# Performance work log

Hardware: AMD Instinct MI355X
Metric: run time of the kernel (lower is better)

The kernel has to match this reference:

```python
import jax, jax.numpy as jnp
import numpy as np

N = 50000      # nodes
E = 1600000    # edges
IN = 128       # in_features
OUT = 64       # out_features
H = 2          # heads
ALPHA = 0.2    # LeakyReLU negative slope


def setup_inputs() -> dict:
    key = jax.random.key(0)
    k1, k2, k3, k4 = jax.random.split(key, 4)
    x = jax.random.normal(k1, (N, IN), dtype=jnp.float32)
    edge_index = jax.random.randint(k2, (2, E), 0, N, dtype=jnp.int32)
    # xavier-uniform-ish scaled params
    W = jax.random.normal(k3, (H, IN, OUT), dtype=jnp.float32) / np.float32(np.sqrt(IN))
    a = jax.random.normal(k4, (H, 2 * OUT, 1), dtype=jnp.float32) * np.float32(0.1)
    return {"x": x, "W": W, "a": a, "edge_index": edge_index}


def reference(x, W, a, edge_index):
    src = edge_index[0]
    dst = edge_index[1]
    # per-head linear transform: [N, H, O]
    Wh = jnp.einsum('ni,hio->nho', x, W)
    # split attention vector: a @ [Wh_i || Wh_j] == Wh_i@a_i + Wh_j@a_j
    a_i = a[:, :OUT, 0]   # [H, O]
    a_j = a[:, OUT:, 0]   # [H, O]
    s_i = jnp.einsum('nho,ho->nh', Wh, a_i)   # [N, H]
    s_j = jnp.einsum('nho,ho->nh', Wh, a_j)   # [N, H]
    # per-edge attention logits, LeakyReLU
    e = jax.nn.leaky_relu(s_i[src] + s_j[dst], negative_slope=ALPHA)  # [E, H]
    # faithful to source: GLOBAL softmax over all edges (dim=0) per head
    attn = jax.nn.softmax(e, axis=0)  # [E, H]
    # dropout with rate 0.0 -> identity (eval mode)
    msg = attn[:, :, None] * Wh[dst]  # [E, H, O]
    h = jax.ops.segment_sum(msg, dst, num_segments=N)  # [N, H, O]
    # concat heads along feature dim
    return h.reshape(N, H * OUT)
```

## Files before the change

### kernel.cpp

```cpp
#include <hip/hip_runtime.h>

#define NN 50000
#define EE 1600000
#define INF 128
#define OUTF 64
#define NH 2
#define ALPHA 0.2f

#define RNG 16
#define NPR (NN / RNG)
#define NBB 250
#define EPB (EE / NBB)
#define BCAP 640
#define NBNODE 391
#define HCH 25
#define SPB (NBB / HCH)

typedef __attribute__((ext_vector_type(8))) short s16x8;
typedef __attribute__((ext_vector_type(4))) float f32x4;

__device__ __forceinline__ unsigned short bf16_rne(float f) {
    union { float f; unsigned u; } v; v.f = f;
    unsigned r = v.u + 0x7FFFu + ((v.u >> 16) & 1u);
    return (unsigned short)(r >> 16);
}
__device__ __forceinline__ float bf16_val(unsigned short h) {
    union { unsigned u; float f; } v; v.u = ((unsigned)h) << 16;
    return v.f;
}
__device__ __forceinline__ void split8(const float4 a, const float4 b,
                                       s16x8& hi, s16x8& lo) {
    const float p[8] = {a.x, a.y, a.z, a.w, b.x, b.y, b.z, b.w};
    #pragma unroll
    for (int j = 0; j < 8; ++j) {
        const unsigned short h = bf16_rne(p[j]);
        hi[j] = (short)h;
        lo[j] = (short)bf16_rne(p[j] - bf16_val(h));
    }
}


__global__ __launch_bounds__(256)
void gat_wprep(const float* __restrict__ Wg, const float* __restrict__ a,
               unsigned short* __restrict__ Wf, float* __restrict__ Z)
{
    const int tid = threadIdx.x;
    const int idx = blockIdx.x * 256 + tid;
    if (idx < 2) Z[idx] = 0.0f;
    {
        const int h = idx >> 13;
        const int k = (idx >> 6) & 127;
        const int o = idx & 63;
        const float w = Wg[idx];
        const unsigned short hi = bf16_rne(w);
        const unsigned short lo = bf16_rne(w - bf16_val(hi));
        const int n  = h * 64 + o;
        const int nt = n >> 4;
        const int ks = k >> 5;
        const int kk = k & 31;
        const int ln = (kk >> 3) * 16 + (n & 15);
        const int pos = ((nt * 4 + ks) * 64 + ln) * 8 + (kk & 7);
        Wf[pos] = hi;
        Wf[18432 + pos] = lo;
    }
    if (blockIdx.x == 0) {
        for (int i = tid; i < 2048; i += 256) {
            Wf[16384 + i] = 0;
            Wf[18432 + 16384 + i] = 0;
        }
        __syncthreads();
        if (tid < 128) {
            const int k = tid;
            float u[4] = {0.f, 0.f, 0.f, 0.f};
            for (int o = 0; o < 64; ++o) {
                const float w0 = Wg[k * 64 + o];
                const float w1 = Wg[8192 + k * 64 + o];
                u[0] = fmaf(w0, a[o], u[0]);
                u[1] = fmaf(w0, a[64 + o], u[1]);
                u[2] = fmaf(w1, a[128 + o], u[2]);
                u[3] = fmaf(w1, a[192 + o], u[3]);
            }
            const int ks = k >> 5;
            const int kk = k & 31;
            #pragma unroll
            for (int n = 0; n < 4; ++n) {
                const int ln = (kk >> 3) * 16 + n;
                const int pos = ((32 + ks) * 64 + ln) * 8 + (kk & 7);
                const unsigned short hi = bf16_rne(u[n]);
                Wf[pos] = hi;
                Wf[18432 + pos] = bf16_rne(u[n] - bf16_val(hi));
            }
        }
    }
}

__global__ __launch_bounds__(256)
void gat_node(const float* __restrict__ x, const unsigned short* __restrict__ Wf,
              const int* __restrict__ ei, float* __restrict__ out,
              float* __restrict__ si, float* __restrict__ sj,
              unsigned* __restrict__ buckets, int* __restrict__ counts)
{
    __shared__ unsigned short WsL[36864];
    __shared__ int cnt[16];
    const int tid = threadIdx.x;

    if (blockIdx.x < NBB) {
        const int bid = blockIdx.x;
        if (tid < 16) cnt[tid] = 0;
        __syncthreads();
        const int e0 = bid * EPB;
        for (int i = tid; i < EPB / 4; i += 256) {
            const int4 s4 = *(const int4*)&ei[e0 + 4 * i];
            const int4 d4 = *(const int4*)&ei[EE + e0 + 4 * i];
            const int ss[4] = {s4.x, s4.y, s4.z, s4.w};
            const int dd[4] = {d4.x, d4.y, d4.z, d4.w};
            #pragma unroll
            for (int k = 0; k < 4; ++k) {
                const int r = dd[k] / NPR;
                const int rel = dd[k] - r * NPR;
                const int pos = atomicAdd(&cnt[r], 1);
                if (pos < BCAP)
                    buckets[(size_t)(r * NBB + bid) * BCAP + pos] =
                        (unsigned)ss[k] | ((unsigned)rel << 16);
            }
        }
        __syncthreads();
        if (tid < 16) counts[tid * NBB + bid] = min(cnt[tid], BCAP);
        return;
    }

    const int bx = blockIdx.x - NBB;
    const int lane = tid & 63;
    const int wv = tid >> 6;
    const int lm = lane & 15;
    const int quad = lane >> 4;

    {
        const float4* gsrc = (const float4*)Wf;
        float4* ldst = (float4*)WsL;
        #pragma unroll
        for (int i = 0; i < 18; ++i)
            ldst[i * 256 + tid] = gsrc[i * 256 + tid];
    }

    const int rowA0 = bx * 128 + wv * 32 + lm;
    const int rowA1 = rowA0 + 16;
    const int rc0 = rowA0 < NN ? rowA0 : NN - 1;
    const int rc1 = rowA1 < NN ? rowA1 : NN - 1;
    const float* xp0 = x + (size_t)rc0 * INF + quad * 8;
    const float* xp1 = x + (size_t)rc1 * INF + quad * 8;

    f32x4 acc[2][9];
    #pragma unroll
    for (int mi = 0; mi < 2; ++mi)
        #pragma unroll
        for (int nt = 0; nt < 9; ++nt) acc[mi][nt] = (f32x4)0.0f;

    __syncthreads();

    #pragma unroll
    for (int ks = 0; ks < 4; ++ks) {
        s16x8 ah0, al0, ah1, al1;
        {
            const float4 u0 = *(const float4*)(xp0 + ks * 32);
            const float4 v0 = *(const float4*)(xp0 + ks * 32 + 4);
            split8(u0, v0, ah0, al0);
            const float4 u1 = *(const float4*)(xp1 + ks * 32);
            const float4 v1 = *(const float4*)(xp1 + ks * 32 + 4);
            split8(u1, v1, ah1, al1);
        }
        #pragma unroll
        for (int nt = 0; nt < 9; ++nt) {
            const s16x8 bh = *(const s16x8*)&WsL[((nt * 4 + ks) * 64 + lane) * 8];
            const s16x8 bl = *(const s16x8*)&WsL[18432 + ((nt * 4 + ks) * 64 + lane) * 8];
            acc[0][nt] = __builtin_amdgcn_mfma_f32_16x16x32_bf16(ah0, bh, acc[0][nt], 0, 0, 0);
            acc[0][nt] = __builtin_amdgcn_mfma_f32_16x16x32_bf16(ah0, bl, acc[0][nt], 0, 0, 0);
            acc[0][nt] = __builtin_amdgcn_mfma_f32_16x16x32_bf16(al0, bh, acc[0][nt], 0, 0, 0);
            acc[1][nt] = __builtin_amdgcn_mfma_f32_16x16x32_bf16(ah1, bh, acc[1][nt], 0, 0, 0);
            acc[1][nt] = __builtin_amdgcn_mfma_f32_16x16x32_bf16(ah1, bl, acc[1][nt], 0, 0, 0);
            acc[1][nt] = __builtin_amdgcn_mfma_f32_16x16x32_bf16(al1, bh, acc[1][nt], 0, 0, 0);
        }
    }

    #pragma unroll
    for (int mi = 0; mi < 2; ++mi) {
        const int rowb = bx * 128 + wv * 32 + mi * 16 + quad * 4;
        #pragma unroll
        for (int r = 0; r < 4; ++r) {
            const int rr = rowb + r;
            if (rr < NN) {
                const float sv = acc[mi][8][r];
                if (lm == 0)      si[2 * rr] = sv;
                else if (lm == 1) sj[2 * rr] = sv;
                else if (lm == 2) si[2 * rr + 1] = sv;
                else if (lm == 3) sj[2 * rr + 1] = sv;
                float* orow = out + (size_t)rr * (NH * OUTF) + lm;
                #pragma unroll
                for (int nt = 0; nt < 8; ++nt) orow[nt * 16] = acc[mi][nt][r];
            }
        }
    }
}

__global__ __launch_bounds__(512)
void gat_hist(const unsigned* __restrict__ buckets, const int* __restrict__ counts,
              const float* __restrict__ si, const float* __restrict__ sj,
              float* __restrict__ partial, float* __restrict__ Z)
{
    __shared__ float bins[NPR * 2];
    __shared__ float zr0[8], zr1[8];
    const int c = blockIdx.x;
    const int r = blockIdx.y;
    const int nlo = r * NPR;

    for (int i = threadIdx.x; i < NPR; i += 512)
        ((float2*)bins)[i] = make_float2(0.f, 0.f);
    __syncthreads();

    float z0 = 0.f, z1 = 0.f;
    #pragma unroll
    for (int bb = 0; bb < SPB; ++bb) {
        const int b = c * SPB + bb;
        const int n = counts[r * NBB + b];
        const uint4* seg4 = (const uint4*)(buckets + (size_t)(r * NBB + b) * BCAP);
        const int n4 = (n + 3) >> 2;
        for (int i = threadIdx.x; i < n4; i += 512) {
            const uint4 pk4 = seg4[i];
            const unsigned pks[4] = {pk4.x, pk4.y, pk4.z, pk4.w};
            #pragma unroll
            for (int j = 0; j < 4; ++j) {
                if (4 * i + j < n) {
                    const unsigned pk = pks[j];
                    const int s = (int)(pk & 0xFFFFu);
                    const int rel = (int)(pk >> 16);
                    const float2 vi = *(const float2*)&si[2 * s];
                    const float2 vj = *(const float2*)&sj[2 * (nlo + rel)];
                    float a0 = vi.x + vj.x; a0 = a0 > 0.f ? a0 : ALPHA * a0;
                    float a1 = vi.y + vj.y; a1 = a1 > 0.f ? a1 : ALPHA * a1;
                    const float w0 = expf(a0);
                    const float w1 = expf(a1);
                    atomicAdd(&bins[2 * rel], w0);
                    atomicAdd(&bins[2 * rel + 1], w1);
                    z0 += w0; z1 += w1;
                }
            }
        }
    }

    #pragma unroll
    for (int m = 1; m < 64; m <<= 1) {
        z0 += __shfl_xor(z0, m, 64);
        z1 += __shfl_xor(z1, m, 64);
    }
    const int wv = threadIdx.x >> 6;
    if ((threadIdx.x & 63) == 0) { zr0[wv] = z0; zr1[wv] = z1; }
    __syncthreads();
    if (threadIdx.x == 0) {
        float t0 = 0.f, t1 = 0.f;
        #pragma unroll
        for (int i = 0; i < 8; ++i) { t0 += zr0[i]; t1 += zr1[i]; }
        atomicAdd(&Z[0], t0);
        atomicAdd(&Z[1], t1);
    }

    float2* P = (float2*)(partial + (size_t)c * 100000 + nlo * 2);
    for (int i = threadIdx.x; i < NPR; i += 512)
        P[i] = ((const float2*)bins)[i];
}

__global__ __launch_bounds__(256)
void gat_scale(float* __restrict__ out, const float* __restrict__ partial,
               const float* __restrict__ Z)
{
    __shared__ float sc[256];
    const int tid = threadIdx.x;
    const int n0 = blockIdx.x * 128;
    const float rz0 = 1.0f / Z[0];
    const float rz1 = 1.0f / Z[1];

    const int nvals = min(256, 100000 - n0 * 2);
    if (tid < nvals) {
        float ssum = 0.f;
        #pragma unroll 5
        for (int c = 0; c < HCH; ++c)
            ssum += partial[(size_t)c * 100000 + n0 * 2 + tid];
        sc[tid] = ssum * ((tid & 1) ? rz1 : rz0);
    }
    __syncthreads();

    float4* ob = (float4*)(out + (size_t)n0 * 128);
    const int lim4 = min(128, NN - n0) * 32;
    for (int i = tid; i < lim4; i += 256) {
        const int row = i >> 5;
        const int c4 = i & 31;
        const float s = sc[row * 2 + (c4 >> 4)];
        float4 v = ob[i];
        v.x *= s; v.y *= s; v.z *= s; v.w *= s;
        ob[i] = v;
    }
}

extern "C" void kernel_launch(void* const* d_in, const int* in_sizes, int n_in,
                              void* d_out, int out_size, void* d_ws, size_t ws_size,
                              hipStream_t stream)
{
    const float* x = (const float*)d_in[0];
    const float* W = (const float*)d_in[1];
    const float* a = (const float*)d_in[2];
    const int* ei = (const int*)d_in[3];
    float* out = (float*)d_out;
    float* ws = (float*)d_ws;

    float* si = ws;
    float* sj = ws + 100000;
    float* Z = ws + 200000;
    unsigned short* Wf = (unsigned short*)(ws + 200016);
    int* counts = (int*)(ws + 218448);
    unsigned* buckets = (unsigned*)(ws + 222464);
    float* partial = ws + 2782464;

    gat_wprep<<<dim3(64), dim3(256), 0, stream>>>(W, a, Wf, Z);

    gat_node<<<dim3(NBB + NBNODE), dim3(256), 0, stream>>>(x, Wf, ei, out, si, sj,
                                                           buckets, counts);

    gat_hist<<<dim3(HCH, RNG), dim3(512), 0, stream>>>(buckets, counts, si, sj,
                                                       partial, Z);

    gat_scale<<<dim3(NBNODE), dim3(256), 0, stream>>>(out, partial, Z);
}
```

Measured before the change: 145.5 us.

## Fuse weight preparation into node kernel and enlarge node blocks

Drops the separate weight-prep kernel. Each node block now splits W into bf16 hi/lo parts, lays it out for MFMA and computes the attention-projected columns directly into LDS. Blocks grow to 512 threads covering 256 rows, which halves the node-block count, and the bucket blocks use the larger stride. This removes one launch and the global round trip for the prepared weights, at the cost of every block redoing the conversion, with scattered LDS stores and a serial 64-step dot product in 128 threads.

```diff
diff --git a/kernel.cpp b/kernel.cpp
--- a/kernel.cpp
+++ b/kernel.cpp
@@ -12,7 +12,7 @@
 #define NBB 250
 #define EPB (EE / NBB)
 #define BCAP 640
-#define NBNODE 391
+#define NBNODE 196
 #define HCH 25
 #define SPB (NBB / HCH)
 
@@ -40,65 +40,12 @@
 }
 
 
-__global__ __launch_bounds__(256)
-void gat_wprep(const float* __restrict__ Wg, const float* __restrict__ a,
-               unsigned short* __restrict__ Wf, float* __restrict__ Z)
-{
-    const int tid = threadIdx.x;
-    const int idx = blockIdx.x * 256 + tid;
-    if (idx < 2) Z[idx] = 0.0f;
-    {
-        const int h = idx >> 13;
-        const int k = (idx >> 6) & 127;
-        const int o = idx & 63;
-        const float w = Wg[idx];
-        const unsigned short hi = bf16_rne(w);
-        const unsigned short lo = bf16_rne(w - bf16_val(hi));
-        const int n  = h * 64 + o;
-        const int nt = n >> 4;
-        const int ks = k >> 5;
-        const int kk = k & 31;
-        const int ln = (kk >> 3) * 16 + (n & 15);
-        const int pos = ((nt * 4 + ks) * 64 + ln) * 8 + (kk & 7);
-        Wf[pos] = hi;
-        Wf[18432 + pos] = lo;
-    }
-    if (blockIdx.x == 0) {
-        for (int i = tid; i < 2048; i += 256) {
-            Wf[16384 + i] = 0;
-            Wf[18432 + 16384 + i] = 0;
-        }
-        __syncthreads();
-        if (tid < 128) {
-            const int k = tid;
-            float u[4] = {0.f, 0.f, 0.f, 0.f};
-            for (int o = 0; o < 64; ++o) {
-                const float w0 = Wg[k * 64 + o];
-                const float w1 = Wg[8192 + k * 64 + o];
-                u[0] = fmaf(w0, a[o], u[0]);
-                u[1] = fmaf(w0, a[64 + o], u[1]);
-                u[2] = fmaf(w1, a[128 + o], u[2]);
-                u[3] = fmaf(w1, a[192 + o], u[3]);
-            }
-            const int ks = k >> 5;
-            const int kk = k & 31;
-            #pragma unroll
-            for (int n = 0; n < 4; ++n) {
-                const int ln = (kk >> 3) * 16 + n;
-                const int pos = ((32 + ks) * 64 + ln) * 8 + (kk & 7);
-                const unsigned short hi = bf16_rne(u[n]);
-                Wf[pos] = hi;
-                Wf[18432 + pos] = bf16_rne(u[n] - bf16_val(hi));
-            }
-        }
-    }
-}
-
-__global__ __launch_bounds__(256)
-void gat_node(const float* __restrict__ x, const unsigned short* __restrict__ Wf,
-              const int* __restrict__ ei, float* __restrict__ out,
-              float* __restrict__ si, float* __restrict__ sj,
-              unsigned* __restrict__ buckets, int* __restrict__ counts)
+__global__ __launch_bounds__(512)
+void gat_node(const float* __restrict__ x, const float* __restrict__ Wg,
+              const float* __restrict__ av, const int* __restrict__ ei,
+              float* __restrict__ out, float* __restrict__ si,
+              float* __restrict__ sj, unsigned* __restrict__ buckets,
+              int* __restrict__ counts, float* __restrict__ Z)
 {
     __shared__ unsigned short WsL[36864];
     __shared__ int cnt[16];
@@ -106,10 +53,11 @@
 
     if (blockIdx.x < NBB) {
         const int bid = blockIdx.x;
+        if (bid == 0 && tid < 2) Z[tid] = 0.0f;
         if (tid < 16) cnt[tid] = 0;
         __syncthreads();
         const int e0 = bid * EPB;
-        for (int i = tid; i < EPB / 4; i += 256) {
+        for (int i = tid; i < EPB / 4; i += 512) {
             const int4 s4 = *(const int4*)&ei[e0 + 4 * i];
             const int4 d4 = *(const int4*)&ei[EE + e0 + 4 * i];
             const int ss[4] = {s4.x, s4.y, s4.z, s4.w};
@@ -135,15 +83,57 @@
     const int lm = lane & 15;
     const int quad = lane >> 4;
 
-    {
-        const float4* gsrc = (const float4*)Wf;
-        float4* ldst = (float4*)WsL;
-        #pragma unroll
-        for (int i = 0; i < 18; ++i)
-            ldst[i * 256 + tid] = gsrc[i * 256 + tid];
-    }
-
-    const int rowA0 = bx * 128 + wv * 32 + lm;
+    for (int idx = tid; idx < 16384; idx += 512) {
+        const int h = idx >> 13;
+        const int k = (idx >> 6) & 127;
+        const int o = idx & 63;
+        const float w = Wg[idx];
+        const unsigned short hi = bf16_rne(w);
+        const unsigned short lo = bf16_rne(w - bf16_val(hi));
+        const int n  = h * 64 + o;
+        const int nt = n >> 4;
+        const int ks = k >> 5;
+        const int kk = k & 31;
+        const int ln = (kk >> 3) * 16 + (n & 15);
+        const int pos = ((nt * 4 + ks) * 64 + ln) * 8 + (kk & 7);
+        WsL[pos] = hi;
+        WsL[18432 + pos] = lo;
+    }
+    for (int i = tid; i < 2048; i += 512) {
+        WsL[16384 + i] = 0;
+        WsL[18432 + 16384 + i] = 0;
+    }
+    __syncthreads();
+    if (tid < 128) {
+        const int k = tid;
+        float u0 = 0.f, u1 = 0.f, u2 = 0.f, u3 = 0.f;
+        #pragma unroll 4
+        for (int o = 0; o < 64; o += 4) {
+            const float4 w0 = *(const float4*)&Wg[k * 64 + o];
+            const float4 w1 = *(const float4*)&Wg[8192 + k * 64 + o];
+            const float4 ai0 = *(const float4*)&av[o];
+            const float4 aj0 = *(const float4*)&av[64 + o];
+            const float4 ai1 = *(const float4*)&av[128 + o];
+            const float4 aj1 = *(const float4*)&av[192 + o];
+            u0 += w0.x*ai0.x + w0.y*ai0.y + w0.z*ai0.z + w0.w*ai0.w;
+            u1 += w0.x*aj0.x + w0.y*aj0.y + w0.z*aj0.z + w0.w*aj0.w;
+            u2 += w1.x*ai1.x + w1.y*ai1.y + w1.z*ai1.z + w1.w*ai1.w;
+            u3 += w1.x*aj1.x + w1.y*aj1.y + w1.z*aj1.z + w1.w*aj1.w;
+        }
+        const float uu[4] = {u0, u1, u2, u3};
+        const int ks = k >> 5;
+        const int kk = k & 31;
+        #pragma unroll
+        for (int n = 0; n < 4; ++n) {
+            const int ln = (kk >> 3) * 16 + n;
+            const int pos = ((32 + ks) * 64 + ln) * 8 + (kk & 7);
+            const unsigned short hi = bf16_rne(uu[n]);
+            WsL[pos] = hi;
+            WsL[18432 + pos] = bf16_rne(uu[n] - bf16_val(hi));
+        }
+    }
+
+    const int rowA0 = bx * 256 + wv * 32 + lm;
     const int rowA1 = rowA0 + 16;
     const int rc0 = rowA0 < NN ? rowA0 : NN - 1;
     const int rc1 = rowA1 < NN ? rowA1 : NN - 1;
@@ -184,7 +174,7 @@
 
     #pragma unroll
     for (int mi = 0; mi < 2; ++mi) {
-        const int rowb = bx * 128 + wv * 32 + mi * 16 + quad * 4;
+        const int rowb = bx * 256 + wv * 32 + mi * 16 + quad * 4;
         #pragma unroll
         for (int r = 0; r < 4; ++r) {
             const int rr = rowb + r;
@@ -314,18 +304,15 @@
     float* si = ws;
     float* sj = ws + 100000;
     float* Z = ws + 200000;
-    unsigned short* Wf = (unsigned short*)(ws + 200016);
-    int* counts = (int*)(ws + 218448);
-    unsigned* buckets = (unsigned*)(ws + 222464);
-    float* partial = ws + 2782464;
-
-    gat_wprep<<<dim3(64), dim3(256), 0, stream>>>(W, a, Wf, Z);
-
-    gat_node<<<dim3(NBB + NBNODE), dim3(256), 0, stream>>>(x, Wf, ei, out, si, sj,
-                                                           buckets, counts);
+    int* counts = (int*)(ws + 200016);
+    unsigned* buckets = (unsigned*)(ws + 204032);
+    float* partial = ws + 2764032;
+
+    gat_node<<<dim3(NBB + NBNODE), dim3(512), 0, stream>>>(x, W, a, ei, out, si, sj,
+                                                           buckets, counts, Z);
 
     gat_hist<<<dim3(HCH, RNG), dim3(512), 0, stream>>>(buckets, counts, si, sj,
                                                        partial, Z);
 
-    gat_scale<<<dim3(NBNODE), dim3(256), 0, stream>>>(out, partial, Z);
-}
+    gat_scale<<<dim3((NN + 127) / 128), dim3(256), 0, stream>>>(out, partial, Z);
+}
```

After: 151.8 us. +4.3%, slower.
